# Optimization experiments

Hardware: AMD Instinct MI355X
Metric: run time of the kernel (lower is better)

Reference implementation:

```python
import jax, jax.numpy as jnp
import numpy as np

SLOW = 32      # LSTM hidden size per weight-neuron
MSG = 16       # message size
MICRO = 2      # micro ticks per layer per step
LAYERS = [(256, 128), (128, 64)]
OUT_IDX = 0
EPS = 1e-6


def _lstm(x, h, c, Wi, Wh, b):
    g = x @ Wi + h @ Wh + b
    i, f, gg, o = jnp.split(g, 4, axis=-1)
    c = jax.nn.sigmoid(f) * c + jax.nn.sigmoid(i) * jnp.tanh(gg)
    h = jax.nn.sigmoid(o) * jnp.tanh(c)
    return h, c


def _ln(x, s, b):
    m = x.mean(-1, keepdims=True)
    v = ((x - m) ** 2).mean(-1, keepdims=True)
    return (x - m) * jax.lax.rsqrt(v + EPS) * s + b


def _merge(state):
    # mean-reduce first half of channels over batch, broadcast back
    half = state.shape[-1] // 2
    s1, s2 = state[..., :half], state[..., half:]
    s1 = jnp.broadcast_to(s1.mean(axis=0, keepdims=True), s1.shape)
    return jnp.concatenate([s1, s2], axis=-1)


def setup_inputs() -> dict:
    key = jax.random.key(0)
    ks = jax.random.split(key, 8)
    T, B = 4, 8
    sc = 0.1
    return {
        "inputs": jax.random.normal(ks[0], (T, B, LAYERS[0][0]), jnp.float32),
        "labels": jax.random.randint(ks[1], (T, B), 0, LAYERS[-1][1]),
        "Wi": jax.random.normal(ks[2], (2 * MSG, 4 * SLOW), jnp.float32) * sc,
        "Wh": jax.random.normal(ks[3], (SLOW, 4 * SLOW), jnp.float32) * sc,
        "b_lstm": jnp.zeros((4 * SLOW,), jnp.float32),
        "Wf": jax.random.normal(ks[4], (SLOW, MSG), jnp.float32) * sc,
        "bf": jnp.zeros((MSG,), jnp.float32),
        "Wb": jax.random.normal(ks[5], (SLOW, MSG), jnp.float32) * sc,
        "bwb": jnp.zeros((MSG,), jnp.float32),
        "ln_fs": jnp.ones((MSG,), jnp.float32),
        "ln_fb": jnp.zeros((MSG,), jnp.float32),
        "ln_bs": jnp.ones((MSG,), jnp.float32),
        "ln_bb": jnp.zeros((MSG,), jnp.float32),
    }


def reference(inputs, labels, Wi, Wh, b_lstm, Wf, bf, Wb, bwb,
              ln_fs, ln_fb, ln_bs, ln_bb):
    T, B, _ = inputs.shape
    n_out = LAYERS[-1][1]
    onehot = jax.nn.one_hot(labels, n_out, dtype=inputs.dtype)

    hs0 = tuple(jnp.zeros((B, i, o, SLOW), inputs.dtype) for i, o in LAYERS)
    cs0 = tuple(jnp.zeros((B, i, o, SLOW), inputs.dtype) for i, o in LAYERS)
    fwd0 = tuple(jnp.zeros((B, i, MSG), inputs.dtype) for i, o in LAYERS)
    bwd0 = tuple(jnp.zeros((B, o, MSG), inputs.dtype) for i, o in LAYERS)
    err0 = jnp.zeros((B, n_out, 2), inputs.dtype)

    def layer(h, c, f, bd):
        # h,c: (B,i,o,S); f: (B,i,M); bd: (B,o,M)
        Bq, ni, no, _ = h.shape
        x = jnp.concatenate([
            jnp.broadcast_to(f[:, :, None, :], (Bq, ni, no, MSG)),
            jnp.broadcast_to(bd[:, None, :, :], (Bq, ni, no, MSG)),
        ], axis=-1)  # (B,i,o,2M)
        for _ in range(MICRO):
            h, c = _lstm(x, h, c, Wi, Wh, b_lstm)
        fm = _ln(h @ Wf + bf, ln_fs, ln_fb)   # (B,i,o,M)
        bm = _ln(h @ Wb + bwb, ln_bs, ln_bb)  # (B,i,o,M)
        return h, c, fm.mean(axis=1), bm.mean(axis=2)

    def step(carry, x):
        hs, cs, fwd, bwd, error = carry
        inp, oh = x
        hs = [_merge(h) for h in hs]
        cs = [_merge(c) for c in cs]
        fwd = list(fwd)
        bwd = list(bwd)
        # inject input into channel 0 of first layer fwd msg
        fwd[0] = jnp.pad(inp[..., None], ((0, 0), (0, 0), (0, MSG - 1)))
        # inject 2-channel error into last layer bwd msg
        bwd[-1] = jnp.pad(error, ((0, 0), (0, 0), (0, MSG - 2)))
        out = None
        for i in range(len(LAYERS)):
            h, c, nf, nb = layer(hs[i], cs[i], fwd[i], bwd[i])
            hs[i], cs[i] = h, c
            if i > 0:
                bwd[i - 1] = nb.reshape(bwd[i - 1].shape)
            if i < len(LAYERS) - 1:
                fwd[i + 1] = nf.reshape(fwd[i + 1].shape)
            else:
                out = nf[..., OUT_IDX]  # (B, n_out)
        grad = jax.nn.softmax(out, axis=-1) - oh  # cross-entropy grad
        new_error = jnp.stack([grad, oh], axis=-1)  # feed_label=True
        return (tuple(hs), tuple(cs), tuple(fwd), tuple(bwd), new_error), out

    carry = (hs0, cs0, fwd0, bwd0, err0)
    _, outputs = jax.lax.scan(step, carry, (inputs, onehot))
    return outputs  # (T, B, n_out)
```

## Files before the change

kernel.cpp:

```cpp
#include <hip/hip_runtime.h>
#include <hip/hip_bf16.h>

#define SLOW 32
#define MSG 16
#define TSTEPS 4
#define BATCH 8
#define NI0 256
#define NO0 128
#define NI1 128
#define NO1 64

typedef __bf16 bf16x8 __attribute__((ext_vector_type(8)));
typedef float f32x4 __attribute__((ext_vector_type(4)));

__device__ __forceinline__ float rcpf(float x) { return __builtin_amdgcn_rcpf(x); }
__device__ __forceinline__ float sigf(float x) { return rcpf(1.f + __expf(-x)); }
__device__ __forceinline__ float tanh_apx(float x) {
    float xc = fminf(fmaxf(x, -15.f), 15.f);
    float e = __expf(-2.f * xc);
    return (1.f - e) * rcpf(1.f + e);
}
__device__ __forceinline__ unsigned short f2bf(float x) {
    __bf16 h = (__bf16)x;
    return __builtin_bit_cast(unsigned short, h);
}
__device__ __forceinline__ float bf2f(unsigned short u) {
    __bf16 h = __builtin_bit_cast(__bf16, u);
    return (float)h;
}
__device__ __forceinline__ float sum16(float v) {
    v += __shfl_xor(v, 1); v += __shfl_xor(v, 2);
    v += __shfl_xor(v, 4); v += __shfl_xor(v, 8);
    return v;
}

__global__ void k_prep(const float* __restrict__ Wh, const float* __restrict__ Wf,
                       const float* __restrict__ Wb, const float* __restrict__ Wi,
                       unsigned short* __restrict__ WhBp,
                       unsigned short* __restrict__ WfBp,
                       unsigned short* __restrict__ WbBp,
                       unsigned short* __restrict__ WiFp) {
    int i = blockIdx.x * 256 + threadIdx.x;
    if (i < 4096) {
        int e = i & 7, l = (i >> 3) & 63, nt = i >> 9;
        int k = (l >> 4) * 8 + e, col = nt * 16 + (l & 15);
        WhBp[i] = f2bf(Wh[k * 128 + col]);
    } else if (i < 4608) {
        int j = i - 4096;
        int e = j & 7, l = j >> 3;
        int k = (l >> 4) * 8 + e;
        WfBp[j] = f2bf(Wf[k * 16 + (l & 15)]);
    } else if (i < 5120) {
        int j = i - 4608;
        int e = j & 7, l = j >> 3;
        int k = (l >> 4) * 8 + e;
        WbBp[j] = f2bf(Wb[k * 16 + (l & 15)]);
    } else if (i < 9216) {
        int j = i - 5120;
        int e = j & 7, l = (j >> 3) & 63, nt = j >> 9;
        int k = (l >> 4) * 8 + e, col = nt * 16 + (l & 15);
        WiFp[j] = (k < 16) ? f2bf(Wi[k * 128 + col]) : (unsigned short)0;
    }
}

__global__ __launch_bounds__(256) void k_l0(
    const float* __restrict__ inp, const float* __restrict__ Wi,
    const unsigned short* __restrict__ WhBp, const float* __restrict__ b_lstm,
    const unsigned short* __restrict__ WfBp, const float* __restrict__ bf_,
    const float* __restrict__ ln_fs, const float* __restrict__ ln_fb,
    unsigned short* __restrict__ h0bf, float* __restrict__ c0g,
    const unsigned short* __restrict__ hm0, const float* __restrict__ cm0,
    const float* __restrict__ nb1, float* __restrict__ nf_part, int t) {
    int q = blockIdx.x & 1;
    int no = (blockIdx.x >> 1) & 127;
    int b = blockIdx.x >> 8;
    int tid = threadIdx.x;
    int w = __builtin_amdgcn_readfirstlane(tid >> 6);
    int l = tid & 63, lo = l & 15, hg = l >> 4;
    const bool wb = (t < TSTEPS - 1);

    __shared__ unsigned short Hbf[128 * 40];
    __shared__ unsigned short BW[4096];
    __shared__ unsigned short BFr[512];
    __shared__ float gsh[128];
    __shared__ float mi_l[128];
    __shared__ float wi0[128];
    __shared__ float redn[4][16];

    {
        unsigned int* d = (unsigned int*)BW;
        const unsigned int* s = (const unsigned int*)WhBp;
#pragma unroll
        for (int i = tid; i < 2048; i += 256) d[i] = s[i];
        ((unsigned int*)BFr)[tid] = ((const unsigned int*)WfBp)[tid];
    }
    if (tid < 128) {
        float acc = b_lstm[tid];
        if (t > 0) {
            const float* nbr = nb1 + ((size_t)b * NO0 + no) * MSG;
#pragma unroll
            for (int m = 0; m < MSG; m++) acc += nbr[m] * Wi[(MSG + m) * 128 + tid];
        }
        gsh[tid] = acc;
        wi0[tid] = Wi[tid];
        mi_l[tid] = inp[((size_t)t * BATCH + b) * NI0 + q * 128 + tid];
    }
    {
        int lc = tid >> 1, half = tid & 1;
        unsigned int* hl = (unsigned int*)Hbf;
        if (t > 0) {
            if (half == 0) {
                const unsigned int* hsrc = (const unsigned int*)hm0 +
                    ((size_t)no * 256 + q * 128 + lc) * 8;
#pragma unroll
                for (int j = 0; j < 8; j++) hl[lc * 20 + j] = hsrc[j];
            } else {
                const unsigned int* hsrc = (const unsigned int*)h0bf +
                    ((size_t)(b * NO0 + no) * 256 + q * 128 + lc) * 16 + 8;
#pragma unroll
                for (int j = 0; j < 8; j++) hl[lc * 20 + 8 + j] = hsrc[j];
            }
        } else {
#pragma unroll
            for (int j = 0; j < 8; j++) hl[lc * 20 + half * 8 + j] = 0u;
        }
    }
    size_t cbase = (size_t)(b * NO0 + no) * 256 * 32;
    float cst[2][4][2];
    if (t > 0) {
#pragma unroll
        for (int mi_ = 0; mi_ < 2; mi_++)
#pragma unroll
            for (int r = 0; r < 4; r++) {
                int gc = q * 128 + (w * 2 + mi_) * 16 + hg * 4 + r;
                cst[mi_][r][0] = cm0[((size_t)no * 256 + gc) * 16 + lo];
                cst[mi_][r][1] = c0g[cbase + (size_t)gc * 32 + lo + 16];
            }
    } else {
#pragma unroll
        for (int mi_ = 0; mi_ < 2; mi_++)
#pragma unroll
            for (int r = 0; r < 4; r++) { cst[mi_][r][0] = 0.f; cst[mi_][r][1] = 0.f; }
    }
    __syncthreads();

    float g8[8], w8[8];
#pragma unroll
    for (int nt = 0; nt < 8; nt++) { g8[nt] = gsh[lo + 16 * nt]; w8[nt] = wi0[lo + 16 * nt]; }
    f32x4 miv[2];
#pragma unroll
    for (int mi_ = 0; mi_ < 2; mi_++)
#pragma unroll
        for (int r = 0; r < 4; r++)
            miv[mi_][r] = mi_l[(w * 2 + mi_) * 16 + hg * 4 + r];

#pragma unroll
    for (int micro = 0; micro < 2; micro++) {
#pragma unroll
        for (int mi_ = 0; mi_ < 2; mi_++) {
            int lt = w * 2 + mi_;
            bf16x8 A = *(const bf16x8*)&Hbf[(lt * 16 + lo) * 40 + hg * 8];
            f32x4 acc[4];
#pragma unroll
            for (int g = 0; g < 4; g++) {
                int nt = 2 * g;
                bf16x8 B = *(const bf16x8*)&BW[(nt * 64 + l) * 8];
                f32x4 ci = g8[nt] + miv[mi_] * w8[nt];
                acc[g] = __builtin_amdgcn_mfma_f32_16x16x32_bf16(A, B, ci, 0, 0, 0);
            }
#pragma unroll
            for (int r = 0; r < 4; r++) {
                int lrow = lt * 16 + hg * 4 + r;
                float cn = sigf(acc[1][r]) * cst[mi_][r][0] + sigf(acc[0][r]) * tanh_apx(acc[2][r]);
                cst[mi_][r][0] = cn;
                float hv = sigf(acc[3][r]) * tanh_apx(cn);
                Hbf[lrow * 40 + lo] = f2bf(hv);
                if (micro == 1 && wb)
                    c0g[cbase + (size_t)(q * 128 + lrow) * 32 + lo] = cn;
            }
#pragma unroll
            for (int g = 0; g < 4; g++) {
                int nt = 2 * g + 1;
                bf16x8 B = *(const bf16x8*)&BW[(nt * 64 + l) * 8];
                f32x4 ci = g8[nt] + miv[mi_] * w8[nt];
                acc[g] = __builtin_amdgcn_mfma_f32_16x16x32_bf16(A, B, ci, 0, 0, 0);
            }
#pragma unroll
            for (int r = 0; r < 4; r++) {
                int lrow = lt * 16 + hg * 4 + r;
                float cn = sigf(acc[1][r]) * cst[mi_][r][1] + sigf(acc[0][r]) * tanh_apx(acc[2][r]);
                cst[mi_][r][1] = cn;
                float hv = sigf(acc[3][r]) * tanh_apx(cn);
                Hbf[lrow * 40 + lo + 16] = f2bf(hv);
                if (micro == 1 && wb)
                    c0g[cbase + (size_t)(q * 128 + lrow) * 32 + lo + 16] = cn;
            }
        }
    }

    bf16x8 Ff = *(const bf16x8*)&BFr[l * 8];
    float lnfs = ln_fs[lo], lnfb = ln_fb[lo];
    float bfv = bf_[lo];
    f32x4 cif = {bfv, bfv, bfv, bfv};
    float nfp = 0.f;
#pragma unroll
    for (int mi_ = 0; mi_ < 2; mi_++) {
        int lt = w * 2 + mi_;
        bf16x8 A = *(const bf16x8*)&Hbf[(lt * 16 + lo) * 40 + hg * 8];
        f32x4 f = __builtin_amdgcn_mfma_f32_16x16x32_bf16(A, Ff, cif, 0, 0, 0);
#pragma unroll
        for (int r = 0; r < 4; r++) {
            float x = f[r];
            float mean = sum16(x) * 0.0625f;
            float d = x - mean;
            float rs = rsqrtf(sum16(d * d) * 0.0625f + 1e-6f);
            nfp += d * rs * lnfs + lnfb;
        }
    }
    nfp += __shfl_xor(nfp, 16);
    nfp += __shfl_xor(nfp, 32);
    if (l < 16) redn[w][l] = nfp;
    __syncthreads();
    if (tid < 16)
        nf_part[(((size_t)b * NO0 + no) * 2 + q) * 16 + tid] =
            redn[0][tid] + redn[1][tid] + redn[2][tid] + redn[3][tid];

    if (wb) {
        int lc = tid >> 1, part = tid & 1;
        unsigned int* hdst =
            (unsigned int*)h0bf +
            ((size_t)(b * NO0 + no) * 256 + q * 128 + lc) * 16 + part * 8;
        const unsigned int* hl = (const unsigned int*)Hbf;
#pragma unroll
        for (int j = 0; j < 8; j++) hdst[j] = hl[lc * 20 + part * 8 + j];
    }
}

__global__ __launch_bounds__(256) void k_l1(
    const float* __restrict__ Wi, const unsigned short* __restrict__ WhBp,
    const float* __restrict__ b_lstm,
    const unsigned short* __restrict__ WfBp, const float* __restrict__ bf_,
    const float* __restrict__ ln_fs, const float* __restrict__ ln_fb,
    const unsigned short* __restrict__ WbBp, const float* __restrict__ bwb,
    const float* __restrict__ ln_bs, const float* __restrict__ ln_bb,
    const unsigned short* __restrict__ WiFp,
    unsigned short* __restrict__ h1bf, float* __restrict__ c1g,
    const unsigned short* __restrict__ hm1, const float* __restrict__ cm1,
    const unsigned short* __restrict__ h0bf, const float* __restrict__ c0g,
    unsigned short* __restrict__ hm0, float* __restrict__ cm0,
    const float* __restrict__ nf_part, const float* __restrict__ gradP,
    const float* __restrict__ ohP,
    float* __restrict__ bm_g, float* __restrict__ outsum_part, int t) {
    int tid = threadIdx.x;
    if (blockIdx.x >= 1024) {
        int mb = blockIdx.x - 1024;
        if (mb < 1024) {
            int idx = mb * 256 + tid;
            int u = idx & 7, cell = (idx >> 3) & 255, no = idx >> 11;
            size_t base = ((size_t)no * 256 + cell) * 16 + u;
            const size_t strd = (size_t)NO0 * 256 * 16;
            const unsigned int* H = (const unsigned int*)h0bf;
            float s0 = 0.f, s1 = 0.f;
#pragma unroll
            for (int b = 0; b < 8; b++) {
                unsigned int v = H[base + b * strd];
                s0 += bf2f((unsigned short)(v & 0xffff));
                s1 += bf2f((unsigned short)(v >> 16));
            }
            ((unsigned int*)hm0)[((size_t)no * 256 + cell) * 8 + u] =
                (unsigned int)f2bf(s0 * 0.125f) | ((unsigned int)f2bf(s1 * 0.125f) << 16);
        } else {
            int idx = (mb - 1024) * 256 + tid;
            int s4 = idx & 3, cell = (idx >> 2) & 255, no = idx >> 10;
            const float4* C = (const float4*)c0g;
            size_t base = ((size_t)no * 256 + cell) * 8 + s4;
            const size_t strd = (size_t)NO0 * 256 * 8;
            float4 a = {0.f, 0.f, 0.f, 0.f};
#pragma unroll
            for (int b = 0; b < 8; b++) {
                float4 v = C[base + b * strd];
                a.x += v.x; a.y += v.y; a.z += v.z; a.w += v.w;
            }
            a.x *= 0.125f; a.y *= 0.125f; a.z *= 0.125f; a.w *= 0.125f;
            ((float4*)cm0)[((size_t)no * 256 + cell) * 4 + s4] = a;
        }
        return;
    }

    int q = blockIdx.x & 1;
    int no = (blockIdx.x >> 1) & 63;
    int b = blockIdx.x >> 7;
    int w = __builtin_amdgcn_readfirstlane(tid >> 6);
    int l = tid & 63, lo = l & 15, hg = l >> 4;
    const bool wb = (t < TSTEPS - 1);

    __shared__ unsigned short Hbf[64 * 40];
    __shared__ unsigned short BW[4096];
    __shared__ unsigned short WiF[4096];
    __shared__ unsigned short BFr[512];
    __shared__ unsigned short BBr[512];
    __shared__ float gsh[128];
    __shared__ float red[4];

    {
        unsigned int* d = (unsigned int*)BW;
        const unsigned int* s = (const unsigned int*)WhBp;
        unsigned int* d2 = (unsigned int*)WiF;
        const unsigned int* s2 = (const unsigned int*)WiFp;
#pragma unroll
        for (int i = tid; i < 2048; i += 256) { d[i] = s[i]; d2[i] = s2[i]; }
        ((unsigned int*)BFr)[tid] = ((const unsigned int*)WfBp)[tid];
        ((unsigned int*)BBr)[tid] = ((const unsigned int*)WbBp)[tid];
    }
    if (tid < 128) {
        float acc = b_lstm[tid];
        if (t > 0) {
            float g = gradP[b * NO1 + no], oh = ohP[b * NO1 + no];
            acc += g * Wi[MSG * 128 + tid] + oh * Wi[(MSG + 1) * 128 + tid];
        }
        gsh[tid] = acc;
    }
    {
        int lc = tid >> 2, part = tid & 3;
        unsigned int* hl = (unsigned int*)Hbf;
        if (t > 0) {
            if (part < 2) {
                const unsigned int* hsrc = (const unsigned int*)hm1 +
                    ((size_t)no * 128 + q * 64 + lc) * 8 + part * 4;
#pragma unroll
                for (int j = 0; j < 4; j++) hl[lc * 20 + part * 4 + j] = hsrc[j];
            } else {
                const unsigned int* hsrc = (const unsigned int*)h1bf +
                    ((size_t)(b * NO1 + no) * 128 + q * 64 + lc) * 16 + part * 4;
#pragma unroll
                for (int j = 0; j < 4; j++) hl[lc * 20 + part * 4 + j] = hsrc[j];
            }
        } else {
#pragma unroll
            for (int j = 0; j < 4; j++) hl[lc * 20 + part * 4 + j] = 0u;
        }
    }
    size_t cbase = (size_t)(b * NO1 + no) * 128 * 32;
    float cst[4][2];
    if (t > 0) {
#pragma unroll
        for (int r = 0; r < 4; r++) {
            int gc = q * 64 + w * 16 + hg * 4 + r;
            cst[r][0] = cm1[((size_t)no * 128 + gc) * 16 + lo];
            cst[r][1] = c1g[cbase + (size_t)gc * 32 + lo + 16];
        }
    } else {
#pragma unroll
        for (int r = 0; r < 4; r++) { cst[r][0] = 0.f; cst[r][1] = 0.f; }
    }
    bf16x8 Anf;
#pragma unroll
    for (int e = 0; e < 8; e++) Anf[e] = (__bf16)0.f;
    if (hg < 2) {
        const float* p = nf_part +
            ((size_t)b * 128 + q * 64 + w * 16 + lo) * 32 + hg * 8;
#pragma unroll
        for (int e = 0; e < 8; e++)
            Anf[e] = (__bf16)((p[e] + p[e + 16]) * (1.f / 256.f));
    }
    __syncthreads();

    f32x4 xf4[8];
    {
        f32x4 zz = {0.f, 0.f, 0.f, 0.f};
#pragma unroll
        for (int nt = 0; nt < 8; nt++) {
            bf16x8 B = *(const bf16x8*)&WiF[(nt * 64 + l) * 8];
            xf4[nt] = __builtin_amdgcn_mfma_f32_16x16x32_bf16(Anf, B, zz, 0, 0, 0);
        }
    }
    float g8[8];
#pragma unroll
    for (int nt = 0; nt < 8; nt++) g8[nt] = gsh[lo + 16 * nt];

#pragma unroll
    for (int micro = 0; micro < 2; micro++) {
        bf16x8 A = *(const bf16x8*)&Hbf[(w * 16 + lo) * 40 + hg * 8];
        f32x4 acc[4];
#pragma unroll
        for (int g = 0; g < 4; g++) {
            int nt = 2 * g;
            bf16x8 B = *(const bf16x8*)&BW[(nt * 64 + l) * 8];
            f32x4 ci = xf4[nt] + g8[nt];
            acc[g] = __builtin_amdgcn_mfma_f32_16x16x32_bf16(A, B, ci, 0, 0, 0);
        }
#pragma unroll
        for (int r = 0; r < 4; r++) {
            float cn = sigf(acc[1][r]) * cst[r][0] + sigf(acc[0][r]) * tanh_apx(acc[2][r]);
            cst[r][0] = cn;
            float hv = sigf(acc[3][r]) * tanh_apx(cn);
            Hbf[(w * 16 + hg * 4 + r) * 40 + lo] = f2bf(hv);
            if (micro == 1 && wb)
                c1g[cbase + (size_t)(q * 64 + w * 16 + hg * 4 + r) * 32 + lo] = cn;
        }
#pragma unroll
        for (int g = 0; g < 4; g++) {
            int nt = 2 * g + 1;
            bf16x8 B = *(const bf16x8*)&BW[(nt * 64 + l) * 8];
            f32x4 ci = xf4[nt] + g8[nt];
            acc[g] = __builtin_amdgcn_mfma_f32_16x16x32_bf16(A, B, ci, 0, 0, 0);
        }
#pragma unroll
        for (int r = 0; r < 4; r++) {
            float cn = sigf(acc[1][r]) * cst[r][1] + sigf(acc[0][r]) * tanh_apx(acc[2][r]);
            cst[r][1] = cn;
            float hv = sigf(acc[3][r]) * tanh_apx(cn);
            Hbf[(w * 16 + hg * 4 + r) * 40 + lo + 16] = f2bf(hv);
            if (micro == 1 && wb)
                c1g[cbase + (size_t)(q * 64 + w * 16 + hg * 4 + r) * 32 + lo + 16] = cn;
        }
    }

    bf16x8 Ff = *(const bf16x8*)&BFr[l * 8];
    float lnfs = ln_fs[lo], lnfb = ln_fb[lo];
    float bfv = bf_[lo];
    f32x4 cif = {bfv, bfv, bfv, bfv};
    float op = 0.f;
    {
        bf16x8 A = *(const bf16x8*)&Hbf[(w * 16 + lo) * 40 + hg * 8];
        f32x4 f = __builtin_amdgcn_mfma_f32_16x16x32_bf16(A, Ff, cif, 0, 0, 0);
#pragma unroll
        for (int r = 0; r < 4; r++) {
            float x = f[r];
            float mean = sum16(x) * 0.0625f;
            float d = x - mean;
            float rs = rsqrtf(sum16(d * d) * 0.0625f + 1e-6f);
            op += d * rs * lnfs + lnfb;
        }
        if (wb) {
            bf16x8 Bb = *(const bf16x8*)&BBr[l * 8];
            float lnbs = ln_bs[lo], lnbb = ln_bb[lo];
            float bwv = bwb[lo];
            f32x4 cib = {bwv, bwv, bwv, bwv};
            f32x4 g = __builtin_amdgcn_mfma_f32_16x16x32_bf16(A, Bb, cib, 0, 0, 0);
#pragma unroll
            for (int r = 0; r < 4; r++) {
                int gc = q * 64 + w * 16 + hg * 4 + r;
                float x = g[r];
                float mean = sum16(x) * 0.0625f;
                float d = x - mean;
                float rs = rsqrtf(sum16(d * d) * 0.0625f + 1e-6f);
                bm_g[(((size_t)b * NO1 + no) * MSG + lo) * NI1 + gc] = d * rs * lnbs + lnbb;
            }
        }
    }
    op += __shfl_xor(op, 16);
    op += __shfl_xor(op, 32);
    if (l == 0) red[w] = op;
    __syncthreads();
    if (tid == 0)
        outsum_part[((size_t)b * NO1 + no) * 2 + q] = red[0] + red[1] + red[2] + red[3];

    if (wb) {
        int lc = tid >> 2, part = tid & 3;
        unsigned int* hdst =
            (unsigned int*)h1bf +
            ((size_t)(b * NO1 + no) * 128 + q * 64 + lc) * 16 + part * 4;
        const unsigned int* hl = (const unsigned int*)Hbf;
#pragma unroll
        for (int j = 0; j < 4; j++) hdst[j] = hl[lc * 20 + part * 4 + j];
    }
}

__global__ __launch_bounds__(256) void k_step_end(
    const unsigned int* __restrict__ h1, const float* __restrict__ c1,
    unsigned short* __restrict__ hm1, float* __restrict__ cm1,
    const float* __restrict__ bm_g, float* __restrict__ nb1,
    const float* __restrict__ outsum_part, const int* __restrict__ labels,
    float* __restrict__ dout, float* __restrict__ gradP,
    float* __restrict__ ohP, int t) {
    int bid = blockIdx.x;
    if (bid < 256) {
        int idx = bid * 256 + threadIdx.x;
        int u = idx & 7, cell = (idx >> 3) & 127, no = idx >> 10;
        size_t base = ((size_t)no * 128 + cell) * 16 + u;
        const size_t strd = (size_t)NO1 * 128 * 16;
        float s0 = 0.f, s1 = 0.f;
#pragma unroll
        for (int b = 0; b < 8; b++) {
            unsigned int v = h1[base + b * strd];
            s0 += bf2f((unsigned short)(v & 0xffff));
            s1 += bf2f((unsigned short)(v >> 16));
        }
        ((unsigned int*)hm1)[((size_t)no * 128 + cell) * 8 + u] =
            (unsigned int)f2bf(s0 * 0.125f) | ((unsigned int)f2bf(s1 * 0.125f) << 16);
        return;
    }
    if (bid < 384) {
        int idx = (bid - 256) * 256 + threadIdx.x;
        int s4 = idx & 3, cell = (idx >> 2) & 127, no = idx >> 9;
        const float4* C = (const float4*)c1;
        size_t base = ((size_t)no * 128 + cell) * 8 + s4;
        const size_t strd = (size_t)NO1 * 128 * 8;
        float4 a = {0.f, 0.f, 0.f, 0.f};
#pragma unroll
        for (int b = 0; b < 8; b++) {
            float4 v = C[base + b * strd];
            a.x += v.x; a.y += v.y; a.z += v.z; a.w += v.w;
        }
        a.x *= 0.125f; a.y *= 0.125f; a.z *= 0.125f; a.w *= 0.125f;
        ((float4*)cm1)[((size_t)no * 128 + cell) * 4 + s4] = a;
        return;
    }
    if (bid < 448) {
        int g = (bid - 384) * 256 + threadIdx.x;
        int ni = g & 127;
        int m = (g >> 7) & 15;
        int b = g >> 11;
        float a = 0.f;
#pragma unroll 8
        for (int no = 0; no < NO1; no++)
            a += bm_g[(((size_t)b * NO1 + no) * MSG + m) * NI1 + ni];
        nb1[((size_t)b * NI1 + ni) * MSG + m] = a * (1.f / NO1);
        return;
    }
    {
        int b = bid - 448;
        int no = threadIdx.x;
        if (no < 64) {
            float v = (outsum_part[((size_t)b * NO1 + no) * 2] +
                       outsum_part[((size_t)b * NO1 + no) * 2 + 1]) * (1.f / 128.f);
            float mx = v;
#pragma unroll
            for (int d = 1; d < 64; d <<= 1) mx = fmaxf(mx, __shfl_xor(mx, d));
            float e = __expf(v - mx);
            float sum = e;
#pragma unroll
            for (int d = 1; d < 64; d <<= 1) sum += __shfl_xor(sum, d);
            int lbl = labels[t * BATCH + b];
            float oh = (no == lbl) ? 1.f : 0.f;
            gradP[b * NO1 + no] = e / sum - oh;
            ohP[b * NO1 + no] = oh;
            dout[((size_t)t * BATCH + b) * NO1 + no] = v;
        }
    }
}

__global__ void k_fin(const float* __restrict__ outsum_part,
                      float* __restrict__ dout) {
    int b = blockIdx.x;
    int no = threadIdx.x;
    float v = (outsum_part[((size_t)b * NO1 + no) * 2] +
               outsum_part[((size_t)b * NO1 + no) * 2 + 1]) * (1.f / 128.f);
    dout[((size_t)(TSTEPS - 1) * BATCH + b) * NO1 + no] = v;
}


extern "C" void kernel_launch(void* const* d_in, const int* in_sizes, int n_in,
                              void* d_out, int out_size, void* d_ws, size_t ws_size,
                              hipStream_t stream) {
    const float* inp   = (const float*)d_in[0];
    const int*   labels= (const int*)d_in[1];
    const float* Wi    = (const float*)d_in[2];
    const float* Wh    = (const float*)d_in[3];
    const float* b_lstm= (const float*)d_in[4];
    const float* Wf    = (const float*)d_in[5];
    const float* bf_   = (const float*)d_in[6];
    const float* Wb    = (const float*)d_in[7];
    const float* bwb   = (const float*)d_in[8];
    const float* ln_fs = (const float*)d_in[9];
    const float* ln_fb = (const float*)d_in[10];
    const float* ln_bs = (const float*)d_in[11];
    const float* ln_bb = (const float*)d_in[12];
    float* out = (float*)d_out;

    const size_t SZ0 = (size_t)BATCH * NO0 * 256 * 32;
    const size_t SZ1 = (size_t)BATCH * NO1 * 128 * 32;

    float* c0 = (float*)d_ws;
    float* c1 = c0 + SZ0;
    unsigned short* h0bf = (unsigned short*)(c1 + SZ1);
    unsigned short* h1bf = h0bf + SZ0;
    float* cm0         = (float*)(h1bf + SZ1);
    float* cm1         = cm0 + 524288;
    unsigned short* hm0 = (unsigned short*)(cm1 + 131072);
    unsigned short* hm1 = hm0 + 524288;
    float* bm_g        = (float*)(hm1 + 131072);
    float* nf_part     = bm_g + 1048576;
    float* nb1         = nf_part + 32768;
    float* outsum_part = nb1 + 16384;
    float* gradP       = outsum_part + 1024;
    float* ohP         = gradP + 512;
    unsigned short* WhBp = (unsigned short*)(ohP + 512);
    unsigned short* WfBp = WhBp + 4096;
    unsigned short* WbBp = WfBp + 512;
    unsigned short* WiFp = WbBp + 512;

    k_prep<<<36, 256, 0, stream>>>(Wh, Wf, Wb, Wi, WhBp, WfBp, WbBp, WiFp);

    for (int t = 0; t < TSTEPS; t++) {
        k_l0<<<BATCH * NO0 * 2, 256, 0, stream>>>(inp, Wi, WhBp, b_lstm, WfBp, bf_,
                                                  ln_fs, ln_fb, h0bf, c0, hm0, cm0,
                                                  nb1, nf_part, t);
        int l1grid = (t < TSTEPS - 1) ? 2560 : 1024;
        k_l1<<<l1grid, 256, 0, stream>>>(Wi, WhBp, b_lstm, WfBp, bf_,
                                         ln_fs, ln_fb, WbBp, bwb, ln_bs, ln_bb,
                                         WiFp, h1bf, c1, hm1, cm1,
                                         h0bf, c0, hm0, cm0,
                                         nf_part, gradP, ohP,
                                         bm_g, outsum_part, t);
        if (t < TSTEPS - 1) {
            k_step_end<<<456, 256, 0, stream>>>((const unsigned int*)h1bf, c1,
                                                hm1, cm1, bm_g, nb1, outsum_part,
                                                labels, out, gradP, ohP, t);
        } else {
            k_fin<<<BATCH, 64, 0, stream>>>(outsum_part, out);
        }
    }
}
```

Measured before the change: 253.6 us.

## Fold layer-1 batch-mean and softmax work into next step's layer-0 kernel

```diff
diff --git a/kernel.cpp b/kernel.cpp
--- a/kernel.cpp
+++ b/kernel.cpp
@@ -63,18 +63,79 @@
     }
 }
 
-__global__ __launch_bounds__(256) void k_l0(
+__global__ __launch_bounds__(256, 6) void k_l0(
     const float* __restrict__ inp, const float* __restrict__ Wi,
     const unsigned short* __restrict__ WhBp, const float* __restrict__ b_lstm,
     const unsigned short* __restrict__ WfBp, const float* __restrict__ bf_,
     const float* __restrict__ ln_fs, const float* __restrict__ ln_fb,
     unsigned short* __restrict__ h0bf, float* __restrict__ c0g,
     const unsigned short* __restrict__ hm0, const float* __restrict__ cm0,
+    const unsigned int* __restrict__ h1bf, const float* __restrict__ c1g,
+    unsigned short* __restrict__ hm1, float* __restrict__ cm1,
+    const float* __restrict__ outsum_part, const int* __restrict__ labels,
+    float* __restrict__ dout, float* __restrict__ gradP, float* __restrict__ ohP,
     const float* __restrict__ nb1, float* __restrict__ nf_part, int t) {
+    int tid = threadIdx.x;
+    if (blockIdx.x >= 2048) {
+        int mb = blockIdx.x - 2048;
+        if (mb < 256) {
+            int idx = mb * 256 + tid;
+            int u = idx & 7, cell = (idx >> 3) & 127, no = idx >> 10;
+            size_t base = ((size_t)no * 128 + cell) * 16 + u;
+            const size_t strd = (size_t)NO1 * 128 * 16;
+            float s0 = 0.f, s1 = 0.f;
+#pragma unroll
+            for (int b = 0; b < 8; b++) {
+                unsigned int v = h1bf[base + b * strd];
+                s0 += bf2f((unsigned short)(v & 0xffff));
+                s1 += bf2f((unsigned short)(v >> 16));
+            }
+            ((unsigned int*)hm1)[((size_t)no * 128 + cell) * 8 + u] =
+                (unsigned int)f2bf(s0 * 0.125f) | ((unsigned int)f2bf(s1 * 0.125f) << 16);
+            return;
+        }
+        if (mb < 384) {
+            int idx = (mb - 256) * 256 + tid;
+            int s4 = idx & 3, cell = (idx >> 2) & 127, no = idx >> 9;
+            const float4* C = (const float4*)c1g;
+            size_t base = ((size_t)no * 128 + cell) * 8 + s4;
+            const size_t strd = (size_t)NO1 * 128 * 8;
+            float4 a = {0.f, 0.f, 0.f, 0.f};
+#pragma unroll
+            for (int b = 0; b < 8; b++) {
+                float4 v = C[base + b * strd];
+                a.x += v.x; a.y += v.y; a.z += v.z; a.w += v.w;
+            }
+            a.x *= 0.125f; a.y *= 0.125f; a.z *= 0.125f; a.w *= 0.125f;
+            ((float4*)cm1)[((size_t)no * 128 + cell) * 4 + s4] = a;
+            return;
+        }
+        {
+            int b = mb - 384;
+            int no = tid;
+            if (no < 64) {
+                float v = (outsum_part[((size_t)b * NO1 + no) * 2] +
+                           outsum_part[((size_t)b * NO1 + no) * 2 + 1]) * (1.f / 128.f);
+                float mx = v;
+#pragma unroll
+                for (int d = 1; d < 64; d <<= 1) mx = fmaxf(mx, __shfl_xor(mx, d));
+                float e = __expf(v - mx);
+                float sum = e;
+#pragma unroll
+                for (int d = 1; d < 64; d <<= 1) sum += __shfl_xor(sum, d);
+                int lbl = labels[(t - 1) * BATCH + b];
+                float oh = (no == lbl) ? 1.f : 0.f;
+                gradP[b * NO1 + no] = e / sum - oh;
+                ohP[b * NO1 + no] = oh;
+                dout[((size_t)(t - 1) * BATCH + b) * NO1 + no] = v;
+            }
+            return;
+        }
+    }
+
     int q = blockIdx.x & 1;
     int no = (blockIdx.x >> 1) & 127;
     int b = blockIdx.x >> 8;
-    int tid = threadIdx.x;
     int w = __builtin_amdgcn_readfirstlane(tid >> 6);
     int l = tid & 63, lo = l & 15, hg = l >> 4;
     const bool wb = (t < TSTEPS - 1);
@@ -467,78 +528,17 @@
     }
 }
 
-__global__ __launch_bounds__(256) void k_step_end(
-    const unsigned int* __restrict__ h1, const float* __restrict__ c1,
-    unsigned short* __restrict__ hm1, float* __restrict__ cm1,
-    const float* __restrict__ bm_g, float* __restrict__ nb1,
-    const float* __restrict__ outsum_part, const int* __restrict__ labels,
-    float* __restrict__ dout, float* __restrict__ gradP,
-    float* __restrict__ ohP, int t) {
-    int bid = blockIdx.x;
-    if (bid < 256) {
-        int idx = bid * 256 + threadIdx.x;
-        int u = idx & 7, cell = (idx >> 3) & 127, no = idx >> 10;
-        size_t base = ((size_t)no * 128 + cell) * 16 + u;
-        const size_t strd = (size_t)NO1 * 128 * 16;
-        float s0 = 0.f, s1 = 0.f;
-#pragma unroll
-        for (int b = 0; b < 8; b++) {
-            unsigned int v = h1[base + b * strd];
-            s0 += bf2f((unsigned short)(v & 0xffff));
-            s1 += bf2f((unsigned short)(v >> 16));
-        }
-        ((unsigned int*)hm1)[((size_t)no * 128 + cell) * 8 + u] =
-            (unsigned int)f2bf(s0 * 0.125f) | ((unsigned int)f2bf(s1 * 0.125f) << 16);
-        return;
-    }
-    if (bid < 384) {
-        int idx = (bid - 256) * 256 + threadIdx.x;
-        int s4 = idx & 3, cell = (idx >> 2) & 127, no = idx >> 9;
-        const float4* C = (const float4*)c1;
-        size_t base = ((size_t)no * 128 + cell) * 8 + s4;
-        const size_t strd = (size_t)NO1 * 128 * 8;
-        float4 a = {0.f, 0.f, 0.f, 0.f};
-#pragma unroll
-        for (int b = 0; b < 8; b++) {
-            float4 v = C[base + b * strd];
-            a.x += v.x; a.y += v.y; a.z += v.z; a.w += v.w;
-        }
-        a.x *= 0.125f; a.y *= 0.125f; a.z *= 0.125f; a.w *= 0.125f;
-        ((float4*)cm1)[((size_t)no * 128 + cell) * 4 + s4] = a;
-        return;
-    }
-    if (bid < 448) {
-        int g = (bid - 384) * 256 + threadIdx.x;
-        int ni = g & 127;
-        int m = (g >> 7) & 15;
-        int b = g >> 11;
-        float a = 0.f;
+__global__ __launch_bounds__(256) void k_nb(const float* __restrict__ bm_g,
+                                            float* __restrict__ nb1) {
+    int g = blockIdx.x * 256 + threadIdx.x;
+    int ni = g & 127;
+    int m = (g >> 7) & 15;
+    int b = g >> 11;
+    float a = 0.f;
 #pragma unroll 8
-        for (int no = 0; no < NO1; no++)
-            a += bm_g[(((size_t)b * NO1 + no) * MSG + m) * NI1 + ni];
-        nb1[((size_t)b * NI1 + ni) * MSG + m] = a * (1.f / NO1);
-        return;
-    }
-    {
-        int b = bid - 448;
-        int no = threadIdx.x;
-        if (no < 64) {
-            float v = (outsum_part[((size_t)b * NO1 + no) * 2] +
-                       outsum_part[((size_t)b * NO1 + no) * 2 + 1]) * (1.f / 128.f);
-            float mx = v;
-#pragma unroll
-            for (int d = 1; d < 64; d <<= 1) mx = fmaxf(mx, __shfl_xor(mx, d));
-            float e = __expf(v - mx);
-            float sum = e;
-#pragma unroll
-            for (int d = 1; d < 64; d <<= 1) sum += __shfl_xor(sum, d);
-            int lbl = labels[t * BATCH + b];
-            float oh = (no == lbl) ? 1.f : 0.f;
-            gradP[b * NO1 + no] = e / sum - oh;
-            ohP[b * NO1 + no] = oh;
-            dout[((size_t)t * BATCH + b) * NO1 + no] = v;
-        }
-    }
+    for (int no = 0; no < NO1; no++)
+        a += bm_g[(((size_t)b * NO1 + no) * MSG + m) * NI1 + ni];
+    nb1[((size_t)b * NI1 + ni) * MSG + m] = a * (1.f / NO1);
 }
 
 __global__ void k_fin(const float* __restrict__ outsum_part,
@@ -594,9 +594,12 @@
     k_prep<<<36, 256, 0, stream>>>(Wh, Wf, Wb, Wi, WhBp, WfBp, WbBp, WiFp);
 
     for (int t = 0; t < TSTEPS; t++) {
-        k_l0<<<BATCH * NO0 * 2, 256, 0, stream>>>(inp, Wi, WhBp, b_lstm, WfBp, bf_,
-                                                  ln_fs, ln_fb, h0bf, c0, hm0, cm0,
-                                                  nb1, nf_part, t);
+        int l0grid = (t > 0) ? 2440 : 2048;
+        k_l0<<<l0grid, 256, 0, stream>>>(inp, Wi, WhBp, b_lstm, WfBp, bf_,
+                                         ln_fs, ln_fb, h0bf, c0, hm0, cm0,
+                                         (const unsigned int*)h1bf, c1, hm1, cm1,
+                                         outsum_part, labels, out, gradP, ohP,
+                                         nb1, nf_part, t);
         int l1grid = (t < TSTEPS - 1) ? 2560 : 1024;
         k_l1<<<l1grid, 256, 0, stream>>>(Wi, WhBp, b_lstm, WfBp, bf_,
                                          ln_fs, ln_fb, WbBp, bwb, ln_bs, ln_bb,
@@ -604,12 +607,8 @@
                                          h0bf, c0, hm0, cm0,
                                          nf_part, gradP, ohP,
                                          bm_g, outsum_part, t);
-        if (t < TSTEPS - 1) {
-            k_step_end<<<456, 256, 0, stream>>>((const unsigned int*)h1bf, c1,
-                                                hm1, cm1, bm_g, nb1, outsum_part,
-                                                labels, out, gradP, ohP, t);
-        } else {
-            k_fin<<<BATCH, 64, 0, stream>>>(outsum_part, out);
-        }
-    }
-}
+        if (t < TSTEPS - 1)
+            k_nb<<<64, 256, 0, stream>>>(bm_g, nb1);
+    }
+    k_fin<<<BATCH, 64, 0, stream>>>(outsum_part, out);
+}
```

Measured after the change: 548.7 us. +116.4%, slower.
